# Kernel optimization log

Hardware: AMD Instinct MI355X
Metric: run time of the kernel (lower is better)

The kernel has to match this reference:

```python
import jax, jax.numpy as jnp
import numpy as np
from jax import lax

# Static configuration (torch module passes these as shape lists / init kwargs)
RATE = 2
FUSE_K = 3
SOFTMAX_SCALE = 10.0
B, L, C = 1, 4096, 64
HS = WS = 64            # downscaled foreground spatial (int_fs)
HB = WB = 64            # background patch grid (int_bs); HB*WB == L
KP = 2 * RATE           # raw patch kernel size = 4
PAD_T = 1               # torch conv_transpose2d padding


def setup_inputs() -> dict:
    key = jax.random.key(0)
    ks = jax.random.split(key, 6)
    raw_w = jax.random.normal(ks[0], (B, L, C, KP, KP), jnp.float32) * 0.1
    mm = (jax.random.uniform(ks[1], (B, L, 1, 1)) > 0.5).astype(jnp.float32)
    scores = jax.random.normal(ks[2], (B, L, HS, WS), jnp.float32)
    w1 = jax.random.normal(ks[3], (C, C, 3, 3), jnp.float32) * 0.05
    b1 = jnp.zeros((C,), jnp.float32)
    w2 = jax.random.normal(ks[4], (C, C, 3, 3), jnp.float32) * 0.05
    b2 = jnp.zeros((C,), jnp.float32)
    return {"raw_w": raw_w, "mm": mm, "scores": scores,
            "w1": w1, "b1": b1, "w2": w2, "b2": b2}


def _conv2d(x, w, b=None, padding=1):
    y = lax.conv_general_dilated(x, w, (1, 1), [(padding, padding)] * 2,
                                 dimension_numbers=('NCHW', 'OIHW', 'NCHW'))
    if b is not None:
        y = y + b[None, :, None, None]
    return y


def _fuse(yi):
    # Diagonal-kernel fusion (DeepFill): treat scores as a (HB*WB) x (HS*WS) image
    # and convolve with an identity (eye) kernel along both pairings.
    k = FUSE_K
    eye = jnp.eye(k, dtype=yi.dtype)[None, None]  # [1,1,k,k]
    x = yi.reshape(B, 1, HB * WB, HS * WS)
    x = _conv2d(x, eye, padding=k // 2)
    x = x.reshape(B, HB, WB, HS, WS).transpose(0, 2, 1, 4, 3)
    x = x.reshape(B, 1, WB * HB, WS * HS)
    x = _conv2d(x, eye, padding=k // 2)
    x = x.reshape(B, WB, HB, WS, HS).transpose(0, 2, 1, 4, 3)  # [B,HB,WB,HS,WS]
    return x.reshape(B, L, HS, WS)


def _deconv_item(y_b, w_b):
    # torch F.conv_transpose2d(y, w, stride=RATE, padding=PAD_T) for one item.
    # y_b: [L,HS,WS], w_b: [L,C,KP,KP] -> [C, RATE*HS, RATE*WS]
    wt = jnp.flip(w_b, axis=(-2, -1)).transpose(1, 0, 2, 3)  # [C,L,KP,KP]
    pad = KP - 1 - PAD_T
    out = lax.conv_general_dilated(y_b[None], wt, (1, 1), [(pad, pad)] * 2,
                                   lhs_dilation=(RATE, RATE),
                                   dimension_numbers=('NCHW', 'OIHW', 'NCHW'))
    return out[0] / 4.0  # overlap normalization (4 = number of overlapping patches)


def reference(raw_w, mm, scores, w1, b1, w2, b2):
    yi = _fuse(scores)
    yi = jax.nn.softmax(yi * mm * SOFTMAX_SCALE, axis=1) * mm  # softmax over L patches
    y = jax.vmap(_deconv_item)(yi, raw_w)  # [B, C, RATE*HS, RATE*WS]
    # trailing Conv+ELU x2 (self.out)
    y = jax.nn.elu(_conv2d(y, w1, b1))
    y = jax.nn.elu(_conv2d(y, w2, b2))
    return y
```

## Files before the change

### kernel.cpp

```cpp
#include <hip/hip_runtime.h>
#include <hip/hip_bf16.h>
#include <hip/hip_fp16.h>
#include <math.h>

#define NL 4096
#define NQ 4096
#define SCALE 10.0f

typedef __bf16 bf16x8 __attribute__((ext_vector_type(8)));
typedef float  f32x4  __attribute__((ext_vector_type(4)));
typedef float  f32x4u __attribute__((ext_vector_type(4), aligned(4)));

#define GLOAD_LDS16(gp, lp)                                                        \
    __builtin_amdgcn_global_load_lds((const __attribute__((address_space(1))) void*)(gp), \
                                     (__attribute__((address_space(3))) void*)(lp), \
                                     16, 0, 0)

__global__ __launch_bounds__(256) void fuseD(const float* __restrict__ S,
                                             float* __restrict__ F) {
    int lin = blockIdx.x;
    int blk = (lin & 7) * 128 + (lin >> 3);
    int l0 = blk * 4;
    int hb = l0 >> 6, wb0 = l0 & 63;
    int tid = threadIdx.x, lane = tid & 63;

    int rowbase[3]; float wm[3][4];
    #pragma unroll
    for (int d = 0; d < 3; ++d) {
        int h2 = hb + d - 1;
        #pragma unroll
        for (int i = 0; i < 4; ++i) wm[d][i] = 1.f;
        if (h2 >= 0 && h2 <= 63) rowbase[d] = h2 * 64 + wb0;
        else if (h2 < 0) {
            rowbase[d] = 4031 + wb0;
            #pragma unroll
            for (int i = 0; i < 4; ++i) wm[d][i] = (wb0 + i >= 1) ? 1.f : 0.f;
        } else {
            rowbase[d] = 1 + wb0;
            #pragma unroll
            for (int i = 0; i < 4; ++i) wm[d][i] = (wb0 + i <= 62) ? 1.f : 0.f;
        }
    }

    for (int cc = 0; cc < 4; ++cc) {
        int q0 = (cc * 256 + tid) * 4;
        int hs = q0 >> 6, ws0 = q0 & 63;
        f32x4 z4 = {0.f, 0.f, 0.f, 0.f};
        f32x4 acc0 = z4, acc1 = z4, acc2 = z4, acc3 = z4;

        #pragma unroll
        for (int d = 0; d < 3; ++d) {
            int s2 = hs + d - 1;
            bool cw = (s2 < 0) || (s2 > 63);
            int colb = cw ? ((s2 < 0 ? 4031 : 1) + ws0) : (q0 + (d - 1) * 64);
            int cb = cw ? colb - 1 : colb;

            f32x4 v[6], v2[6];
            #pragma unroll
            for (int r = 0; r < 6; ++r) {
                int rr = rowbase[d] - 1 + r;
                v[r] = z4;
                if (rr >= 0 && rr < 4096)
                    v[r] = *(const f32x4u*)(S + (size_t)rr * 4096 + cb);
            }
            if (cw) {
                #pragma unroll
                for (int r = 0; r < 6; ++r) {
                    int rr = rowbase[d] - 1 + r;
                    v2[r] = z4;
                    if (rr >= 0 && rr < 4096)
                        v2[r] = *(const f32x4u*)(S + (size_t)rr * 4096 + colb + 1);
                }
            }

            float lm[4], rm[4];
            #pragma unroll
            for (int r = 0; r < 4; ++r) lm[r] = __shfl_up(v[r][3], 1);
            #pragma unroll
            for (int r = 0; r < 4; ++r) rm[r] = __shfl_down(v[r + 2][0], 1);
            if (!cw) {
                if (lane == 0 || colb == 0) {
                    #pragma unroll
                    for (int r = 0; r < 4; ++r) {
                        int rr = rowbase[d] - 1 + r;
                        lm[r] = (colb > 0 && rr >= 0 && rr < 4096)
                                ? S[(size_t)rr * 4096 + colb - 1] : 0.f;
                    }
                }
                if (lane == 63 || colb + 4 >= 4096) {
                    #pragma unroll
                    for (int r = 0; r < 4; ++r) {
                        int rr = rowbase[d] + 1 + r;
                        rm[r] = (colb + 4 < 4096 && rr >= 0 && rr < 4096)
                                ? S[(size_t)rr * 4096 + colb + 4] : 0.f;
                    }
                }
            }

            f32x4 t[4];
            if (!cw) {
                #pragma unroll
                for (int i = 0; i < 4; ++i) {
                    f32x4 Lv = { lm[i], v[i][0], v[i][1], v[i][2] };
                    f32x4 Cv = v[i + 1];
                    f32x4 Rv = { v[i + 2][1], v[i + 2][2], v[i + 2][3], rm[i] };
                    t[i] = Lv + Cv + Rv;
                }
            } else {
                #pragma unroll
                for (int i = 0; i < 4; ++i) {
                    f32x4 Lv = v[i];
                    f32x4 Cv = { v[i+1][1], v[i+1][2], v[i+1][3], v2[i+1][2] };
                    f32x4 Rv = v2[i + 2];
                    t[i] = Lv + Cv + Rv;
                }
                if (s2 < 0 && ws0 == 0) { t[0][0] = 0.f; t[1][0] = 0.f; t[2][0] = 0.f; t[3][0] = 0.f; }
                if (s2 > 63 && ws0 == 60) { t[0][3] = 0.f; t[1][3] = 0.f; t[2][3] = 0.f; t[3][3] = 0.f; }
            }
            acc0 += wm[d][0] * t[0];
            acc1 += wm[d][1] * t[1];
            acc2 += wm[d][2] * t[2];
            acc3 += wm[d][3] * t[3];
        }
        *(f32x4*)(F + (size_t)(l0 + 0) * 4096 + q0) = acc0;
        *(f32x4*)(F + (size_t)(l0 + 1) * 4096 + q0) = acc1;
        *(f32x4*)(F + (size_t)(l0 + 2) * 4096 + q0) = acc2;
        *(f32x4*)(F + (size_t)(l0 + 3) * 4096 + q0) = acc3;
    }
}

__global__ __launch_bounds__(256) void softPart(const float* __restrict__ F,
                                                const float* __restrict__ mm,
                                                float* __restrict__ Pm,
                                                float* __restrict__ Ps) {
    int qt = blockIdx.x, lc = blockIdx.y;
    int qo = threadIdx.x & 63, lg = threadIdx.x >> 6;
    int q = qt * 64 + qo;
    __shared__ float red[4][64];

    float sv[32];
    float m = -1e30f;
    #pragma unroll
    for (int i = 0; i < 32; ++i) {
        int l = lc * 128 + i * 4 + lg;
        float s = F[(size_t)l * 4096 + q] * mm[l] * SCALE;
        sv[i] = s;
        m = fmaxf(m, s);
    }
    red[lg][qo] = m;
    __syncthreads();
    m = fmaxf(fmaxf(red[0][qo], red[1][qo]), fmaxf(red[2][qo], red[3][qo]));
    __syncthreads();

    float sum = 0.f;
    #pragma unroll
    for (int i = 0; i < 32; ++i) sum += __expf(sv[i] - m);
    red[lg][qo] = sum;
    __syncthreads();
    if (lg == 0) {
        sum = red[0][qo] + red[1][qo] + red[2][qo] + red[3][qo];
        Pm[lc * 4096 + q] = m;
        Ps[lc * 4096 + q] = sum;
    }
}

__global__ void softComb(const float* __restrict__ Pm, const float* __restrict__ Ps,
                         float* __restrict__ Qm, float* __restrict__ Qi) {
    int q = blockIdx.x * 256 + threadIdx.x;
    float M = -1e30f;
    #pragma unroll
    for (int i = 0; i < 32; ++i) M = fmaxf(M, Pm[i * 4096 + q]);
    float S = 0.f;
    #pragma unroll
    for (int i = 0; i < 32; ++i) S += Ps[i * 4096 + q] * __expf(Pm[i * 4096 + q] - M);
    Qm[q] = M;
    Qi[q] = 1.0f / S;
}

__global__ __launch_bounds__(256) void normTransP(const float* __restrict__ F,
                                                  const float* __restrict__ mm,
                                                  const float* __restrict__ Qm,
                                                  const float* __restrict__ Qi,
                                                  __hip_bfloat16* __restrict__ Pt) {
    __shared__ float T[64][65];
    int qt = blockIdx.x, lt = blockIdx.y;
    int t = threadIdx.x;
    int lq = t >> 4;
    int q4 = (t & 15) * 4;
    float4 qm4 = *(const float4*)&Qm[qt * 64 + q4];
    float4 qi4 = *(const float4*)&Qi[qt * 64 + q4];

    #pragma unroll
    for (int p = 0; p < 4; ++p) {
        int l = p * 16 + lq;
        float mml = mm[lt * 64 + l];
        f32x4 v = *(const f32x4*)&F[(size_t)(lt * 64 + l) * 4096 + qt * 64 + q4];
        T[l][q4 + 0] = mml * __expf(v[0] * mml * SCALE - qm4.x) * qi4.x;
        T[l][q4 + 1] = mml * __expf(v[1] * mml * SCALE - qm4.y) * qi4.y;
        T[l][q4 + 2] = mml * __expf(v[2] * mml * SCALE - qm4.z) * qi4.z;
        T[l][q4 + 3] = mml * __expf(v[3] * mml * SCALE - qm4.w) * qi4.w;
    }
    __syncthreads();

    int l4 = (t & 15) * 4;
    #pragma unroll
    for (int p = 0; p < 4; ++p) {
        int ql = p * 16 + (t >> 4);
        __hip_bfloat16 ob[4];
        #pragma unroll
        for (int i = 0; i < 4; ++i) ob[i] = (__hip_bfloat16)T[l4 + i][ql];
        *(uint2*)&Pt[(size_t)(qt * 64 + ql) * 4096 + lt * 64 + l4] = *(const uint2*)ob;
    }
}

__global__ __launch_bounds__(256) void transW(const float* __restrict__ Wsrc,
                                              __hip_bfloat16* __restrict__ Wt) {
    __shared__ float T[64][65];
    int nt = blockIdx.x, kt = blockIdx.y;
    int c = threadIdx.x & 63;
    #pragma unroll
    for (int p = 0; p < 16; ++p) {
        int r = p * 4 + (threadIdx.x >> 6);
        T[r][c] = Wsrc[(size_t)(kt * 64 + r) * 1024 + nt * 64 + c];
    }
    __syncthreads();
    #pragma unroll
    for (int p = 0; p < 16; ++p) {
        int r = p * 4 + (threadIdx.x >> 6);
        int n_new = (r & 15) * 64 + nt * 4 + (r >> 4);
        Wt[(size_t)n_new * 4096 + kt * 64 + c] = (__hip_bfloat16)T[c][r];
    }
}

__global__ void transWc(const float* __restrict__ Wsrc, __hip_bfloat16* __restrict__ Wd) {
    int t = blockIdx.x * 256 + threadIdx.x;
    int kyx = t >> 12;
    int co = (t >> 6) & 63;
    int ci = t & 63;
    Wd[t] = (__hip_bfloat16)Wsrc[co * 576 + ci * 9 + kyx];
}

__global__ __launch_bounds__(256) void gemmMfmaK(const __hip_bfloat16* __restrict__ Ab,
                                                 const __hip_bfloat16* __restrict__ Bb,
                                                 __half* __restrict__ C0,
                                                 __half* __restrict__ C1,
                                                 __half* __restrict__ C2,
                                                 __half* __restrict__ C3) {
    __shared__ __align__(16) __hip_bfloat16 As[2][128][32];
    __shared__ __align__(16) __hip_bfloat16 Bs[2][128][32];
    int lin = blockIdx.x;
    int wid = (lin & 7) * 128 + (lin >> 3);
    int bz = wid >> 8;
    int r5 = wid & 255;
    int bn = r5 & 7;
    int bm = r5 >> 3;
    int bm0 = bm * 128, bn0 = bn * 128;
    size_t kbase = (size_t)bz * 1024;
    __half* Cm = (bz == 0) ? C0 : (bz == 1) ? C1 : (bz == 2) ? C2 : C3;

    int tid = threadIdx.x;
    int lane = tid & 63, w = tid >> 6;
    int wm = (w >> 1) * 64, wn = (w & 1) * 64;

    int srow = w * 32 + (lane >> 2);
    int scol = (((lane & 3) ^ ((lane >> 3) & 3))) * 8;
    const __hip_bfloat16* ga0 = Ab + (size_t)(bm0 + srow) * 4096 + kbase + scol;
    const __hip_bfloat16* ga1 = Ab + (size_t)(bm0 + srow + 16) * 4096 + kbase + scol;
    const __hip_bfloat16* gb0 = Bb + (size_t)(bn0 + srow) * 4096 + kbase + scol;
    const __hip_bfloat16* gb1 = Bb + (size_t)(bn0 + srow + 16) * 4096 + kbase + scol;

    f32x4 acc[4][4] = {};
    int fm = lane & 15;
    int fkz = (((lane >> 4) ^ ((lane >> 1) & 3))) * 8;

    GLOAD_LDS16(ga0, &As[0][w * 32][0]);
    GLOAD_LDS16(ga1, &As[0][w * 32 + 16][0]);
    GLOAD_LDS16(gb0, &Bs[0][w * 32][0]);
    GLOAD_LDS16(gb1, &Bs[0][w * 32 + 16][0]);
    __syncthreads();

    int buf = 0;
    for (int t = 0; t < 32; ++t) {
        if (t + 1 < 32) {
            int k0 = (t + 1) * 32;
            GLOAD_LDS16(ga0 + k0, &As[buf ^ 1][w * 32][0]);
            GLOAD_LDS16(ga1 + k0, &As[buf ^ 1][w * 32 + 16][0]);
            GLOAD_LDS16(gb0 + k0, &Bs[buf ^ 1][w * 32][0]);
            GLOAD_LDS16(gb1 + k0, &Bs[buf ^ 1][w * 32 + 16][0]);
        }
        bf16x8 af[4], bfr[4];
        #pragma unroll
        for (int i = 0; i < 4; ++i)
            af[i] = *(const bf16x8*)&As[buf][wm + i * 16 + fm][fkz];
        #pragma unroll
        for (int j = 0; j < 4; ++j)
            bfr[j] = *(const bf16x8*)&Bs[buf][wn + j * 16 + fm][fkz];
        #pragma unroll
        for (int i = 0; i < 4; ++i)
            #pragma unroll
            for (int j = 0; j < 4; ++j)
                acc[i][j] = __builtin_amdgcn_mfma_f32_16x16x32_bf16(af[i], bfr[j], acc[i][j], 0, 0, 0);
        __syncthreads();
        buf ^= 1;
    }

    #pragma unroll
    for (int i = 0; i < 4; ++i) {
        #pragma unroll
        for (int j = 0; j < 4; ++j) {
            int row = bm0 + wm + i * 16 + (lane >> 4) * 4;
            int col = bn0 + wn + j * 16 + (lane & 15);
            #pragma unroll
            for (int r = 0; r < 4; ++r)
                Cm[(size_t)(row + r) * 1024 + col] = __float2half(acc[i][j][r]);
        }
    }
}

__global__ void scatterD(const __half* __restrict__ Mo, const __half* __restrict__ Mo2,
                         const __half* __restrict__ Mo3, const __half* __restrict__ Mo4,
                         __hip_bfloat16* __restrict__ Xp) {
    int c = threadIdx.x & 63;
    int pix = blockIdx.x * 4 + (threadIdx.x >> 6);
    int ox = pix & 127, oy = pix >> 7;
    float acc = 0.f;
    #pragma unroll
    for (int ky = 0; ky < 4; ++ky) {
        int ty = oy + 1 - ky;
        if (ty & 1) continue;
        int iy = ty >> 1;
        if (iy < 0 || iy >= 64) continue;
        #pragma unroll
        for (int kx = 0; kx < 4; ++kx) {
            int txx = ox + 1 - kx;
            if (txx & 1) continue;
            int ix = txx >> 1;
            if (ix < 0 || ix >= 64) continue;
            size_t off = (size_t)(iy * 64 + ix) * 1024 + (ky * 4 + kx) * 64 + c;
            acc += (__half2float(Mo[off]) + __half2float(Mo2[off]))
                 + (__half2float(Mo3[off]) + __half2float(Mo4[off]));
        }
    }
    Xp[((size_t)(oy + 1) * 130 + ox + 1) * 64 + c] = (__hip_bfloat16)(acc * 0.25f);
}

template <int MODE>
__global__ __launch_bounds__(256) void convMfma(const __hip_bfloat16* __restrict__ Xp,
                                                const __hip_bfloat16* __restrict__ Wc,
                                                const float* __restrict__ Bi,
                                                __hip_bfloat16* __restrict__ Yp,
                                                float* __restrict__ Yo) {
    int tid = threadIdx.x, lane = tid & 63, w = tid >> 6;
    int y = blockIdx.x >> 1, x0 = (blockIdx.x & 1) * 64;
    int co0 = w * 16;
    int fl = lane & 15, fh = lane >> 4;

    bf16x8 wb[3][3][2];
    #pragma unroll
    for (int ky = 0; ky < 3; ++ky)
        #pragma unroll
        for (int kx = 0; kx < 3; ++kx)
            #pragma unroll
            for (int kc = 0; kc < 2; ++kc)
                wb[ky][kx][kc] = *(const bf16x8*)&Wc[(size_t)((ky * 3 + kx) * 64 + co0 + fl) * 64 + kc * 32 + fh * 8];

    f32x4 acc[4] = {};
    #pragma unroll
    for (int ky = 0; ky < 3; ++ky) {
        #pragma unroll
        for (int kx = 0; kx < 3; ++kx) {
            const __hip_bfloat16* xrow = Xp + ((size_t)(y + ky) * 130 + x0 + kx) * 64;
            #pragma unroll
            for (int kc = 0; kc < 2; ++kc) {
                #pragma unroll
                for (int mt = 0; mt < 4; ++mt) {
                    bf16x8 af = *(const bf16x8*)&xrow[(mt * 16 + fl) * 64 + kc * 32 + fh * 8];
                    acc[mt] = __builtin_amdgcn_mfma_f32_16x16x32_bf16(af, wb[ky][kx][kc], acc[mt], 0, 0, 0);
                }
            }
        }
    }

    float bias = Bi[co0 + fl];
    #pragma unroll
    for (int mt = 0; mt < 4; ++mt) {
        int xb = x0 + mt * 16 + fh * 4;
        if (MODE == 0) {
            #pragma unroll
            for (int r = 0; r < 4; ++r) {
                float v = acc[mt][r] + bias;
                v = v > 0.f ? v : expm1f(v);
                Yp[((size_t)(y + 1) * 130 + xb + r + 1) * 64 + co0 + fl] = (__hip_bfloat16)v;
            }
        } else {
            float4 o;
            float* op = (float*)&o;
            #pragma unroll
            for (int r = 0; r < 4; ++r) {
                float v = acc[mt][r] + bias;
                op[r] = v > 0.f ? v : expm1f(v);
            }
            *(float4*)&Yo[(size_t)(co0 + fl) * 16384 + y * 128 + xb] = o;
        }
    }
}

extern "C" void kernel_launch(void* const* d_in, const int* in_sizes, int n_in,
                              void* d_out, int out_size, void* d_ws, size_t ws_size,
                              hipStream_t stream) {
    const float* raw_w  = (const float*)d_in[0];
    const float* mm     = (const float*)d_in[1];
    const float* scores = (const float*)d_in[2];
    const float* w1     = (const float*)d_in[3];
    const float* b1     = (const float*)d_in[4];
    const float* w2     = (const float*)d_in[5];
    const float* b2     = (const float*)d_in[6];
    float* out = (float*)d_out;

    char* ws = (char*)d_ws;
    __hip_bfloat16* Pt  = (__hip_bfloat16*)ws;
    __hip_bfloat16* Wt  = (__hip_bfloat16*)(ws + (32ull << 20));
    float*          Pm  = (float*)(ws + (40ull << 20));
    float*          Ps  = (float*)(ws + (40ull << 20) + (512u << 10));
    float*          Qm  = (float*)(ws + (41ull << 20));
    float*          Qi  = (float*)(ws + (41ull << 20) + (64u << 10));
    __hip_bfloat16* Wc1 = (__hip_bfloat16*)(ws + (41ull << 20) + (256u << 10));
    __hip_bfloat16* Wc2 = (__hip_bfloat16*)(ws + (41ull << 20) + (384u << 10));
    __half*         Mo  = (__half*)(ws + (42ull << 20));
    __half*         Mo2 = (__half*)(ws + (50ull << 20));
    __hip_bfloat16* Xp  = (__hip_bfloat16*)(ws + (58ull << 20));
    __hip_bfloat16* Y1p = (__hip_bfloat16*)(ws + (61ull << 20));
    float*          F   = (float*)(ws + (64ull << 20));
    __half*         Mo3 = (__half*)(ws + (64ull << 20));
    __half*         Mo4 = (__half*)(ws + (72ull << 20));

    const size_t XP_BYTES = 130ull * 130 * 64 * sizeof(__hip_bfloat16);

    fuseD<<<1024, 256, 0, stream>>>(scores, F);
    transW<<<dim3(16, 64), 256, 0, stream>>>(raw_w, Wt);
    transWc<<<144, 256, 0, stream>>>(w1, Wc1);
    transWc<<<144, 256, 0, stream>>>(w2, Wc2);
    softPart<<<dim3(64, 32), 256, 0, stream>>>(F, mm, Pm, Ps);
    softComb<<<16, 256, 0, stream>>>(Pm, Ps, Qm, Qi);
    normTransP<<<dim3(64, 64), 256, 0, stream>>>(F, mm, Qm, Qi, Pt);
    gemmMfmaK<<<1024, 256, 0, stream>>>(Pt, Wt, Mo, Mo2, Mo3, Mo4);
    hipMemsetAsync(Xp, 0, XP_BYTES, stream);
    hipMemsetAsync(Y1p, 0, XP_BYTES, stream);
    scatterD<<<4096, 256, 0, stream>>>(Mo, Mo2, Mo3, Mo4, Xp);
    convMfma<0><<<256, 256, 0, stream>>>(Xp, Wc1, b1, Y1p, nullptr);
    convMfma<1><<<256, 256, 0, stream>>>(Y1p, Wc2, b2, nullptr, out);
}
```

Before: 166.7 us.

## Write fused scores transposed and replace three-pass softmax with per-row kernel

The fusion kernel now computes 16 patches per thread and writes its output transposed through shared memory, so each query's scores over all patches are contiguous. A single row-softmax kernel then reads one row per block, reduces max and sum with wave shuffles, and writes normalized bf16 probabilities directly. This replaces the partial-softmax, combine and normalize-transpose kernels. Full memsets of the padded conv buffers are replaced by a small kernel that zeroes only the border pixels. The larger per-thread register footprint in the fusion kernel may lower its occupancy, and the border-only zeroing assumes the scatter fills the interior.

New measurement: 173.6 us. 4.1% more time.

```diff
diff --git a/kernel.cpp b/kernel.cpp
--- a/kernel.cpp
+++ b/kernel.cpp
@@ -16,200 +16,176 @@
                                      (__attribute__((address_space(3))) void*)(lp), \
                                      16, 0, 0)
 
-__global__ __launch_bounds__(256) void fuseD(const float* __restrict__ S,
-                                             float* __restrict__ F) {
-    int lin = blockIdx.x;
-    int blk = (lin & 7) * 128 + (lin >> 3);
-    int l0 = blk * 4;
-    int hb = l0 >> 6, wb0 = l0 & 63;
+__global__ __launch_bounds__(256) void fuseDT(const float* __restrict__ S,
+                                              float* __restrict__ Ft) {
+    int bx = blockIdx.x;
+    int lg = (bx & 7) * 32 + (bx >> 3);
+    int l0 = lg * 16;
+    int hb = l0 >> 6;
+    int wb0 = l0 & 63;
     int tid = threadIdx.x, lane = tid & 63;
-
-    int rowbase[3]; float wm[3][4];
+    int qbase = blockIdx.y * 1024;
+    int q0 = qbase + tid * 4;
+    int hs = q0 >> 6, ws0 = q0 & 63;
+
+    f32x4 z4 = {0.f, 0.f, 0.f, 0.f};
+    f32x4 acc[16];
+    #pragma unroll
+    for (int i = 0; i < 16; ++i) acc[i] = z4;
+
     #pragma unroll
     for (int d = 0; d < 3; ++d) {
         int h2 = hb + d - 1;
-        #pragma unroll
-        for (int i = 0; i < 4; ++i) wm[d][i] = 1.f;
-        if (h2 >= 0 && h2 <= 63) rowbase[d] = h2 * 64 + wb0;
-        else if (h2 < 0) {
-            rowbase[d] = 4031 + wb0;
-            #pragma unroll
-            for (int i = 0; i < 4; ++i) wm[d][i] = (wb0 + i >= 1) ? 1.f : 0.f;
-        } else {
-            rowbase[d] = 1 + wb0;
-            #pragma unroll
-            for (int i = 0; i < 4; ++i) wm[d][i] = (wb0 + i <= 62) ? 1.f : 0.f;
-        }
-    }
-
-    for (int cc = 0; cc < 4; ++cc) {
-        int q0 = (cc * 256 + tid) * 4;
-        int hs = q0 >> 6, ws0 = q0 & 63;
-        f32x4 z4 = {0.f, 0.f, 0.f, 0.f};
-        f32x4 acc0 = z4, acc1 = z4, acc2 = z4, acc3 = z4;
-
-        #pragma unroll
-        for (int d = 0; d < 3; ++d) {
-            int s2 = hs + d - 1;
-            bool cw = (s2 < 0) || (s2 > 63);
-            int colb = cw ? ((s2 < 0 ? 4031 : 1) + ws0) : (q0 + (d - 1) * 64);
-            int cb = cw ? colb - 1 : colb;
-
-            f32x4 v[6], v2[6];
-            #pragma unroll
-            for (int r = 0; r < 6; ++r) {
-                int rr = rowbase[d] - 1 + r;
-                v[r] = z4;
+        int rowbase;
+        if (h2 >= 0 && h2 <= 63) rowbase = h2 * 64 + wb0;
+        else if (h2 < 0)         rowbase = 4031 + wb0;
+        else                     rowbase = 1 + wb0;
+        bool skip0  = (h2 < 0)  && (wb0 == 0);
+        bool skip15 = (h2 > 63) && (wb0 == 48);
+
+        int s2 = hs + d - 1;
+        bool cw = (s2 < 0) || (s2 > 63);
+        int colb = cw ? ((s2 < 0 ? 4031 : 1) + ws0) : (q0 + (d - 1) * 64);
+        int cb = cw ? colb - 1 : colb;
+
+        f32x4 v[18], v2[18];
+        #pragma unroll
+        for (int r = 0; r < 18; ++r) {
+            int rr = rowbase - 1 + r;
+            v[r] = z4;
+            if (rr >= 0 && rr < 4096)
+                v[r] = *(const f32x4u*)(S + (size_t)rr * 4096 + cb);
+        }
+        if (cw) {
+            #pragma unroll
+            for (int r = 0; r < 18; ++r) {
+                int rr = rowbase - 1 + r;
+                v2[r] = z4;
                 if (rr >= 0 && rr < 4096)
-                    v[r] = *(const f32x4u*)(S + (size_t)rr * 4096 + cb);
-            }
-            if (cw) {
+                    v2[r] = *(const f32x4u*)(S + (size_t)rr * 4096 + colb + 1);
+            }
+        }
+
+        float lm[16], rm[16];
+        #pragma unroll
+        for (int r = 0; r < 16; ++r) lm[r] = __shfl_up(v[r][3], 1);
+        #pragma unroll
+        for (int r = 0; r < 16; ++r) rm[r] = __shfl_down(v[r + 2][0], 1);
+        if (!cw) {
+            if (lane == 0 || colb == 0) {
                 #pragma unroll
-                for (int r = 0; r < 6; ++r) {
-                    int rr = rowbase[d] - 1 + r;
-                    v2[r] = z4;
-                    if (rr >= 0 && rr < 4096)
-                        v2[r] = *(const f32x4u*)(S + (size_t)rr * 4096 + colb + 1);
+                for (int r = 0; r < 16; ++r) {
+                    int rr = rowbase - 1 + r;
+                    lm[r] = (colb > 0 && rr >= 0 && rr < 4096)
+                            ? S[(size_t)rr * 4096 + colb - 1] : 0.f;
                 }
             }
-
-            float lm[4], rm[4];
-            #pragma unroll
-            for (int r = 0; r < 4; ++r) lm[r] = __shfl_up(v[r][3], 1);
-            #pragma unroll
-            for (int r = 0; r < 4; ++r) rm[r] = __shfl_down(v[r + 2][0], 1);
+            if (lane == 63 || colb + 4 >= 4096) {
+                #pragma unroll
+                for (int r = 0; r < 16; ++r) {
+                    int rr = rowbase + 1 + r;
+                    rm[r] = (colb + 4 < 4096 && rr >= 0 && rr < 4096)
+                            ? S[(size_t)rr * 4096 + colb + 4] : 0.f;
+                }
+            }
+        }
+
+        #pragma unroll
+        for (int i = 0; i < 16; ++i) {
+            f32x4 ti;
             if (!cw) {
-                if (lane == 0 || colb == 0) {
-                    #pragma unroll
-                    for (int r = 0; r < 4; ++r) {
-                        int rr = rowbase[d] - 1 + r;
-                        lm[r] = (colb > 0 && rr >= 0 && rr < 4096)
-                                ? S[(size_t)rr * 4096 + colb - 1] : 0.f;
-                    }
-                }
-                if (lane == 63 || colb + 4 >= 4096) {
-                    #pragma unroll
-                    for (int r = 0; r < 4; ++r) {
-                        int rr = rowbase[d] + 1 + r;
-                        rm[r] = (colb + 4 < 4096 && rr >= 0 && rr < 4096)
-                                ? S[(size_t)rr * 4096 + colb + 4] : 0.f;
-                    }
-                }
-            }
-
-            f32x4 t[4];
-            if (!cw) {
-                #pragma unroll
-                for (int i = 0; i < 4; ++i) {
-                    f32x4 Lv = { lm[i], v[i][0], v[i][1], v[i][2] };
-                    f32x4 Cv = v[i + 1];
-                    f32x4 Rv = { v[i + 2][1], v[i + 2][2], v[i + 2][3], rm[i] };
-                    t[i] = Lv + Cv + Rv;
-                }
+                f32x4 Lv = { lm[i], v[i][0], v[i][1], v[i][2] };
+                f32x4 Cv = v[i + 1];
+                f32x4 Rv = { v[i + 2][1], v[i + 2][2], v[i + 2][3], rm[i] };
+                ti = Lv + Cv + Rv;
             } else {
-                #pragma unroll
-                for (int i = 0; i < 4; ++i) {
-                    f32x4 Lv = v[i];
-                    f32x4 Cv = { v[i+1][1], v[i+1][2], v[i+1][3], v2[i+1][2] };
-                    f32x4 Rv = v2[i + 2];
-                    t[i] = Lv + Cv + Rv;
-                }
-                if (s2 < 0 && ws0 == 0) { t[0][0] = 0.f; t[1][0] = 0.f; t[2][0] = 0.f; t[3][0] = 0.f; }
-                if (s2 > 63 && ws0 == 60) { t[0][3] = 0.f; t[1][3] = 0.f; t[2][3] = 0.f; t[3][3] = 0.f; }
-            }
-            acc0 += wm[d][0] * t[0];
-            acc1 += wm[d][1] * t[1];
-            acc2 += wm[d][2] * t[2];
-            acc3 += wm[d][3] * t[3];
-        }
-        *(f32x4*)(F + (size_t)(l0 + 0) * 4096 + q0) = acc0;
-        *(f32x4*)(F + (size_t)(l0 + 1) * 4096 + q0) = acc1;
-        *(f32x4*)(F + (size_t)(l0 + 2) * 4096 + q0) = acc2;
-        *(f32x4*)(F + (size_t)(l0 + 3) * 4096 + q0) = acc3;
-    }
-}
-
-__global__ __launch_bounds__(256) void softPart(const float* __restrict__ F,
-                                                const float* __restrict__ mm,
-                                                float* __restrict__ Pm,
-                                                float* __restrict__ Ps) {
-    int qt = blockIdx.x, lc = blockIdx.y;
-    int qo = threadIdx.x & 63, lg = threadIdx.x >> 6;
-    int q = qt * 64 + qo;
-    __shared__ float red[4][64];
-
-    float sv[32];
+                f32x4 Lv = v[i];
+                f32x4 Cv = { v[i+1][1], v[i+1][2], v[i+1][3], v2[i+1][2] };
+                f32x4 Rv = v2[i + 2];
+                ti = Lv + Cv + Rv;
+                if (s2 < 0 && ws0 == 0)   ti[0] = 0.f;
+                if (s2 > 63 && ws0 == 60) ti[3] = 0.f;
+            }
+            bool skip = (i == 0 && skip0) || (i == 15 && skip15);
+            if (!skip) acc[i] += ti;
+        }
+    }
+
+    __shared__ float T[16][260];
+    int sg = tid >> 6;
+    #pragma unroll
+    for (int st = 0; st < 4; ++st) {
+        if (sg == st) {
+            int qc = (tid & 63) * 4;
+            #pragma unroll
+            for (int i = 0; i < 16; ++i)
+                *(f32x4*)&T[i][qc] = acc[i];
+        }
+        __syncthreads();
+        {
+            float tmp[16];
+            #pragma unroll
+            for (int i = 0; i < 16; ++i) tmp[i] = T[i][tid];
+            float* dst = Ft + (size_t)(qbase + st * 256 + tid) * 4096 + l0;
+            #pragma unroll
+            for (int i2 = 0; i2 < 4; ++i2) {
+                f32x4 o = { tmp[i2*4], tmp[i2*4+1], tmp[i2*4+2], tmp[i2*4+3] };
+                *(f32x4*)&dst[i2 * 4] = o;
+            }
+        }
+        __syncthreads();
+    }
+}
+
+__global__ __launch_bounds__(256) void rowSoftmax(const float* __restrict__ Ft,
+                                                  const float* __restrict__ mm,
+                                                  __hip_bfloat16* __restrict__ Pt) {
+    int q = blockIdx.x;
+    int tid = threadIdx.x, lane = tid & 63, w = tid >> 6;
+    const float4* Fr = (const float4*)(Ft + (size_t)q * 4096);
+    const float4* M4 = (const float4*)mm;
+    __shared__ float red[4];
+
+    float sv[4][4], mv[4][4];
     float m = -1e30f;
     #pragma unroll
-    for (int i = 0; i < 32; ++i) {
-        int l = lc * 128 + i * 4 + lg;
-        float s = F[(size_t)l * 4096 + q] * mm[l] * SCALE;
-        sv[i] = s;
-        m = fmaxf(m, s);
-    }
-    red[lg][qo] = m;
+    for (int c = 0; c < 4; ++c) {
+        int i = c * 256 + tid;
+        float4 f = Fr[i], g = M4[i];
+        #pragma unroll
+        for (int j = 0; j < 4; ++j) {
+            float s = ((const float*)&f)[j] * ((const float*)&g)[j] * SCALE;
+            sv[c][j] = s;
+            mv[c][j] = ((const float*)&g)[j];
+            m = fmaxf(m, s);
+        }
+    }
+    #pragma unroll
+    for (int off = 32; off >= 1; off >>= 1) m = fmaxf(m, __shfl_xor(m, off));
+    if (lane == 0) red[w] = m;
     __syncthreads();
-    m = fmaxf(fmaxf(red[0][qo], red[1][qo]), fmaxf(red[2][qo], red[3][qo]));
+    m = fmaxf(fmaxf(red[0], red[1]), fmaxf(red[2], red[3]));
     __syncthreads();
 
     float sum = 0.f;
     #pragma unroll
-    for (int i = 0; i < 32; ++i) sum += __expf(sv[i] - m);
-    red[lg][qo] = sum;
+    for (int c = 0; c < 4; ++c)
+        #pragma unroll
+        for (int j = 0; j < 4; ++j) sum += __expf(sv[c][j] - m);
+    #pragma unroll
+    for (int off = 32; off >= 1; off >>= 1) sum += __shfl_xor(sum, off);
+    if (lane == 0) red[w] = sum;
     __syncthreads();
-    if (lg == 0) {
-        sum = red[0][qo] + red[1][qo] + red[2][qo] + red[3][qo];
-        Pm[lc * 4096 + q] = m;
-        Ps[lc * 4096 + q] = sum;
-    }
-}
-
-__global__ void softComb(const float* __restrict__ Pm, const float* __restrict__ Ps,
-                         float* __restrict__ Qm, float* __restrict__ Qi) {
-    int q = blockIdx.x * 256 + threadIdx.x;
-    float M = -1e30f;
-    #pragma unroll
-    for (int i = 0; i < 32; ++i) M = fmaxf(M, Pm[i * 4096 + q]);
-    float S = 0.f;
-    #pragma unroll
-    for (int i = 0; i < 32; ++i) S += Ps[i * 4096 + q] * __expf(Pm[i * 4096 + q] - M);
-    Qm[q] = M;
-    Qi[q] = 1.0f / S;
-}
-
-__global__ __launch_bounds__(256) void normTransP(const float* __restrict__ F,
-                                                  const float* __restrict__ mm,
-                                                  const float* __restrict__ Qm,
-                                                  const float* __restrict__ Qi,
-                                                  __hip_bfloat16* __restrict__ Pt) {
-    __shared__ float T[64][65];
-    int qt = blockIdx.x, lt = blockIdx.y;
-    int t = threadIdx.x;
-    int lq = t >> 4;
-    int q4 = (t & 15) * 4;
-    float4 qm4 = *(const float4*)&Qm[qt * 64 + q4];
-    float4 qi4 = *(const float4*)&Qi[qt * 64 + q4];
-
-    #pragma unroll
-    for (int p = 0; p < 4; ++p) {
-        int l = p * 16 + lq;
-        float mml = mm[lt * 64 + l];
-        f32x4 v = *(const f32x4*)&F[(size_t)(lt * 64 + l) * 4096 + qt * 64 + q4];
-        T[l][q4 + 0] = mml * __expf(v[0] * mml * SCALE - qm4.x) * qi4.x;
-        T[l][q4 + 1] = mml * __expf(v[1] * mml * SCALE - qm4.y) * qi4.y;
-        T[l][q4 + 2] = mml * __expf(v[2] * mml * SCALE - qm4.z) * qi4.z;
-        T[l][q4 + 3] = mml * __expf(v[3] * mml * SCALE - qm4.w) * qi4.w;
-    }
-    __syncthreads();
-
-    int l4 = (t & 15) * 4;
-    #pragma unroll
-    for (int p = 0; p < 4; ++p) {
-        int ql = p * 16 + (t >> 4);
+    float inv = 1.0f / (red[0] + red[1] + red[2] + red[3]);
+
+    #pragma unroll
+    for (int c = 0; c < 4; ++c) {
+        int i = c * 256 + tid;
         __hip_bfloat16 ob[4];
         #pragma unroll
-        for (int i = 0; i < 4; ++i) ob[i] = (__hip_bfloat16)T[l4 + i][ql];
-        *(uint2*)&Pt[(size_t)(qt * 64 + ql) * 4096 + lt * 64 + l4] = *(const uint2*)ob;
+        for (int j = 0; j < 4; ++j)
+            ob[j] = (__hip_bfloat16)(mv[c][j] * __expf(sv[c][j] - m) * inv);
+        *(uint2*)(Pt + (size_t)q * 4096 + i * 4) = *(const uint2*)ob;
     }
 }
 
@@ -238,6 +214,19 @@
     int co = (t >> 6) & 63;
     int ci = t & 63;
     Wd[t] = (__hip_bfloat16)Wsrc[co * 576 + ci * 9 + kyx];
+}
+
+__global__ void zeroB(__hip_bfloat16* __restrict__ Xp, __hip_bfloat16* __restrict__ Y1p) {
+    int p = blockIdx.x;
+    int c = threadIdx.x;
+    int y, x;
+    if (p < 130)      { y = 0;   x = p; }
+    else if (p < 260) { y = 129; x = p - 130; }
+    else if (p < 388) { y = p - 260 + 1; x = 0; }
+    else              { y = p - 388 + 1; x = 129; }
+    size_t off = ((size_t)y * 130 + x) * 64 + c;
+    Xp[off]  = (__hip_bfloat16)0.f;
+    Y1p[off] = (__hip_bfloat16)0.f;
 }
 
 __global__ __launch_bounds__(256) void gemmMfmaK(const __hip_bfloat16* __restrict__ Ab,
@@ -420,32 +409,23 @@
     char* ws = (char*)d_ws;
     __hip_bfloat16* Pt  = (__hip_bfloat16*)ws;
     __hip_bfloat16* Wt  = (__hip_bfloat16*)(ws + (32ull << 20));
-    float*          Pm  = (float*)(ws + (40ull << 20));
-    float*          Ps  = (float*)(ws + (40ull << 20) + (512u << 10));
-    float*          Qm  = (float*)(ws + (41ull << 20));
-    float*          Qi  = (float*)(ws + (41ull << 20) + (64u << 10));
     __hip_bfloat16* Wc1 = (__hip_bfloat16*)(ws + (41ull << 20) + (256u << 10));
     __hip_bfloat16* Wc2 = (__hip_bfloat16*)(ws + (41ull << 20) + (384u << 10));
     __half*         Mo  = (__half*)(ws + (42ull << 20));
     __half*         Mo2 = (__half*)(ws + (50ull << 20));
     __hip_bfloat16* Xp  = (__hip_bfloat16*)(ws + (58ull << 20));
     __hip_bfloat16* Y1p = (__hip_bfloat16*)(ws + (61ull << 20));
-    float*          F   = (float*)(ws + (64ull << 20));
+    float*          Ft  = (float*)(ws + (64ull << 20));
     __half*         Mo3 = (__half*)(ws + (64ull << 20));
     __half*         Mo4 = (__half*)(ws + (72ull << 20));
 
-    const size_t XP_BYTES = 130ull * 130 * 64 * sizeof(__hip_bfloat16);
-
-    fuseD<<<1024, 256, 0, stream>>>(scores, F);
+    fuseDT<<<dim3(256, 4), 256, 0, stream>>>(scores, Ft);
     transW<<<dim3(16, 64), 256, 0, stream>>>(raw_w, Wt);
     transWc<<<144, 256, 0, stream>>>(w1, Wc1);
     transWc<<<144, 256, 0, stream>>>(w2, Wc2);
-    softPart<<<dim3(64, 32), 256, 0, stream>>>(F, mm, Pm, Ps);
-    softComb<<<16, 256, 0, stream>>>(Pm, Ps, Qm, Qi);
-    normTransP<<<dim3(64, 64), 256, 0, stream>>>(F, mm, Qm, Qi, Pt);
+    zeroB<<<516, 64, 0, stream>>>(Xp, Y1p);
+    rowSoftmax<<<4096, 256, 0, stream>>>(Ft, mm, Pt);
     gemmMfmaK<<<1024, 256, 0, stream>>>(Pt, Wt, Mo, Mo2, Mo3, Mo4);
-    hipMemsetAsync(Xp, 0, XP_BYTES, stream);
-    hipMemsetAsync(Y1p, 0, XP_BYTES, stream);
     scatterD<<<4096, 256, 0, stream>>>(Mo, Mo2, Mo3, Mo4, Xp);
     convMfma<0><<<256, 256, 0, stream>>>(Xp, Wc1, b1, Y1p, nullptr);
     convMfma<1><<<256, 256, 0, stream>>>(Y1p, Wc2, b2, nullptr, out);
```
